# Kernel optimization log

Measured on AMD Instinct MI355X. Metric: run time of the kernel, lower is better.

Reference implementation:

```python
import jax, jax.numpy as jnp
import numpy as np

D_MODEL = 1024
H = 16
D_K = D_MODEL // H
NEG = -1e9


def setup_inputs() -> dict:
    key = jax.random.key(0)
    ks = jax.random.split(key, 12)
    B, S = 4, 2048
    scale = 1.0 / np.sqrt(D_MODEL)
    return {
        "q": jax.random.normal(ks[0], (B, S, D_MODEL), dtype=jnp.float32),
        "k": jax.random.normal(ks[1], (B, S, D_MODEL), dtype=jnp.float32),
        "v": jax.random.normal(ks[2], (B, S, D_MODEL), dtype=jnp.float32),
        "mask": jnp.ones((1, 1, S, S), dtype=jnp.int32),
        "w_q": jax.random.normal(ks[3], (D_MODEL, D_MODEL), dtype=jnp.float32) * scale,
        "b_q": jnp.zeros((D_MODEL,), dtype=jnp.float32),
        "w_k": jax.random.normal(ks[4], (D_MODEL, D_MODEL), dtype=jnp.float32) * scale,
        "b_k": jnp.zeros((D_MODEL,), dtype=jnp.float32),
        "w_v": jax.random.normal(ks[5], (D_MODEL, D_MODEL), dtype=jnp.float32) * scale,
        "b_v": jnp.zeros((D_MODEL,), dtype=jnp.float32),
        "w_o": jax.random.normal(ks[6], (D_MODEL, D_MODEL), dtype=jnp.float32) * scale,
        "b_o": jnp.zeros((D_MODEL,), dtype=jnp.float32),
    }


def reference(q, k, v, mask, w_q, b_q, w_k, b_k, w_v, b_v, w_o, b_o):
    B, S, _ = q.shape
    # projections (torch Linear: x @ W^T + b)
    query = q @ w_q.T + b_q
    key = k @ w_k.T + b_k
    value = v @ w_v.T + b_v
    # [B, S, D] -> [B, H, S, d_k]
    query = query.reshape(B, S, H, D_K).transpose(0, 2, 1, 3)
    key = key.reshape(B, S, H, D_K).transpose(0, 2, 1, 3)
    value = value.reshape(B, S, H, D_K).transpose(0, 2, 1, 3)
    # scaled dot-product attention, full [B,H,S,S] scores as in original
    scores = jnp.einsum("bhqd,bhkd->bhqk", query, key) / jnp.sqrt(
        jnp.asarray(D_K, dtype=query.dtype)
    )
    scores = jnp.where(mask == 0, jnp.asarray(NEG, dtype=scores.dtype), scores)
    attn = jax.nn.softmax(scores, axis=-1)
    x = jnp.einsum("bhqk,bhkd->bhqd", attn, value)
    # [B, H, S, d_k] -> [B, S, D]
    x = x.transpose(0, 2, 1, 3).reshape(B, S, H * D_K)
    return x @ w_o.T + b_o
```

## Files before the change

kernel.cpp:

```cpp
#include <hip/hip_runtime.h>

typedef unsigned short u16;
typedef unsigned int u32;
typedef unsigned long long u64;
typedef __attribute__((ext_vector_type(8))) short short8;
typedef __attribute__((ext_vector_type(4))) float f32x4;
typedef __attribute__((ext_vector_type(16))) float f32x16;
typedef __attribute__((ext_vector_type(4))) u32 u32x4;

constexpr int S_LEN = 2048;
constexpr int DMODEL = 1024;

#if __has_builtin(__builtin_amdgcn_exp2f)
#define EXP2 __builtin_amdgcn_exp2f
#else
#define EXP2 exp2f
#endif

__device__ __forceinline__ u16 f2bf(float f) {
  u32 u = __builtin_bit_cast(u32, f);
  u += 0x7FFFu + ((u >> 16) & 1u);
  return (u16)(u >> 16);
}

__device__ __forceinline__ u32 cvtpk(float a, float b) {
  u32 r;
  asm("v_cvt_pk_bf16_f32 %0, %1, %2" : "=v"(r) : "v"(a), "v"(b));
  return r;
}

__device__ __forceinline__ void plswap(u32& a, u32& b) {
  asm("v_permlane32_swap_b32 %0, %1" : "+v"(a), "+v"(b));
}

__device__ __forceinline__ void gload_lds16(const void* g, void* l) {
  __builtin_amdgcn_global_load_lds((const __attribute__((address_space(1))) u32*)g,
                                   (__attribute__((address_space(3))) u32*)l,
                                   16, 0, 0);
}

__global__ __launch_bounds__(256) void prep_kernel(
    const float* __restrict__ w0, const float* __restrict__ w1,
    const float* __restrict__ w2, const float* __restrict__ w3,
    u16* __restrict__ o0, u16* __restrict__ o1,
    u16* __restrict__ o2, u16* __restrict__ o3,
    const int* __restrict__ mask, u64* __restrict__ mb) {
  if (blockIdx.y == 4) {
    int gw = (blockIdx.x * 256 + threadIdx.x) >> 6;
    int lane = threadIdx.x & 63;
    #pragma unroll
    for (int i = 0; i < 16; ++i) {
      size_t word = (size_t)gw * 16 + i;
      int m = mask[word * 64 + lane];
      u64 bits = __ballot(m != 0);
      if (lane == 0) mb[word] = bits;
    }
    return;
  }
  const float* src; u16* dst;
  switch (blockIdx.y) {
    case 0: src = w0; dst = o0; break;
    case 1: src = w1; dst = o1; break;
    case 2: src = w2; dst = o2; break;
    default: src = w3; dst = o3; break;
  }
  int i = blockIdx.x * 256 + threadIdx.x;
  float4 v = ((const float4*)src)[i];
  ushort4 h;
  h.x = f2bf(v.x); h.y = f2bf(v.y); h.z = f2bf(v.z); h.w = f2bf(v.w);
  ((ushort4*)dst)[i] = h;
}

__global__ __launch_bounds__(256) void cvt_a3_kernel(
    const float* __restrict__ s0, const float* __restrict__ s1,
    const float* __restrict__ s2,
    u16* __restrict__ d0, u16* __restrict__ d1, u16* __restrict__ d2) {
  const float* src; u16* dst;
  switch (blockIdx.y) {
    case 0: src = s0; dst = d0; break;
    case 1: src = s1; dst = d1; break;
    default: src = s2; dst = d2; break;
  }
  int i = blockIdx.x * 256 + threadIdx.x;
  float4 v = ((const float4*)src)[i];
  ushort4 h;
  h.x = f2bf(v.x); h.y = f2bf(v.y); h.z = f2bf(v.z); h.w = f2bf(v.w);
  ((ushort4*)dst)[i] = h;
}

template<int OM>
__global__ __launch_bounds__(256) void gemm_bt_kernel(
    const u16* __restrict__ A, const u16* __restrict__ W,
    const float* __restrict__ bias, void* __restrict__ Cv, float scale) {
  constexpr int BK = 32;
  __shared__ __align__(16) u16 As[128 * BK];
  __shared__ __align__(16) u16 Bs[128 * BK];
  const int tid = threadIdx.x;
  const int lane = tid & 63, w = tid >> 6;
  const int l15 = lane & 15, lg = lane >> 4;
  const int m0 = blockIdx.x * 128, n0 = blockIdx.y * 128;
  const int wm = w >> 1, wn = w & 1;
  f32x4 acc[4][4] = {};

  for (int kt = 0; kt < 1024; kt += BK) {
    #pragma unroll
    for (int j = 0; j < 2; ++j) {
      int sb = (w * 2 + j) * 64;
      int slot = sb + lane;
      int row = slot >> 2, c8 = slot & 3;
      gload_lds16(W + (size_t)(n0 + row) * 1024 + kt + c8 * 8,
                  (char*)Bs + (size_t)sb * 16);
      gload_lds16(A + (size_t)(m0 + row) * 1024 + kt + c8 * 8,
                  (char*)As + (size_t)sb * 16);
    }
    __syncthreads();
    short8 af[4], bfr[4];
    #pragma unroll
    for (int m = 0; m < 4; ++m)
      af[m] = *(const short8*)&As[(wm * 64 + m * 16 + l15) * BK + lg * 8];
    #pragma unroll
    for (int n = 0; n < 4; ++n)
      bfr[n] = *(const short8*)&Bs[(wn * 64 + n * 16 + l15) * BK + lg * 8];
    #pragma unroll
    for (int m = 0; m < 4; ++m)
      #pragma unroll
      for (int n = 0; n < 4; ++n)
        acc[m][n] = __builtin_amdgcn_mfma_f32_16x16x32_bf16(af[m], bfr[n], acc[m][n], 0, 0, 0);
    __syncthreads();
  }

  #pragma unroll
  for (int m = 0; m < 4; ++m) {
    #pragma unroll
    for (int n = 0; n < 4; ++n) {
      int col = n0 + wn * 64 + n * 16 + l15;
      float bcol = bias[col];
      int row0 = m0 + wm * 64 + m * 16 + lg * 4;
      if constexpr (OM == 2) {
        int b = row0 >> 11, s = row0 & 2047;
        ushort4 o;
        o.x = f2bf((acc[m][n][0] + bcol) * scale);
        o.y = f2bf((acc[m][n][1] + bcol) * scale);
        o.z = f2bf((acc[m][n][2] + bcol) * scale);
        o.w = f2bf((acc[m][n][3] + bcol) * scale);
        u16* dst = (u16*)Cv + ((size_t)(b * 16 + (col >> 6)) * 64 + (col & 63)) * S_LEN + s;
        *(ushort4*)dst = o;
      } else {
        #pragma unroll
        for (int r = 0; r < 4; ++r) {
          float v = (acc[m][n][r] + bcol) * scale;
          if constexpr (OM == 1)
            ((float*)Cv)[(size_t)(row0 + r) * 1024 + col] = v;
          else
            ((u16*)Cv)[(size_t)(row0 + r) * 1024 + col] = f2bf(v);
        }
      }
    }
  }
}

__global__ __launch_bounds__(256, 4) void attn_kernel(
    const u16* __restrict__ Qp, const u16* __restrict__ Kp,
    const u16* __restrict__ VpT, const u64* __restrict__ mb,
    u16* __restrict__ X) {
  constexpr float NEGL2 = -1.4426950e9f;
  __shared__ __align__(16) u16 Ks[2][4096];
  __shared__ __align__(16) u16 VTs[2][4096];
  const int tid = threadIdx.x;
  const int lane = tid & 63, w = tid >> 6;
  const int l31 = lane & 31, hi1 = lane >> 5;

  u32 id = blockIdx.x;
  u32 nid = ((id & 7) << 7) | (id >> 3);
  const int bh = nid >> 4, qt = nid & 15;
  const int b = bh >> 4, h = bh & 15;
  const size_t bS = (size_t)b * S_LEN;
  const int wq0 = qt * 128 + w * 32;

  short8 qf[4];
  {
    const u16* qb = Qp + (bS + wq0 + l31) * DMODEL + h * 64;
    #pragma unroll
    for (int dk = 0; dk < 4; ++dk)
      qf[dk] = *(const short8*)(qb + dk * 16 + hi1 * 8);
  }

  f32x16 xacc[2] = {};
  float lsum = 0.f;

  auto stage = [&](int k0, int nb) {
    #pragma unroll
    for (int i = 0; i < 2; ++i) {
      int g = tid + i * 256;
      int kk = g >> 3, dh = g & 7;
      gload_lds16(Kp + (bS + k0 + kk) * DMODEL + h * 64 + ((dh ^ (kk & 7)) << 3),
                  (char*)&Ks[nb][0] + g * 16);
    }
    #pragma unroll
    for (int i = 0; i < 2; ++i) {
      int g = tid + i * 256;
      int dd = g >> 3, kh = g & 7;
      gload_lds16(VpT + ((size_t)(bh * 64 + dd)) * S_LEN + k0 + ((kh ^ (dd & 7)) << 3),
                  (char*)&VTs[nb][0] + g * 16);
    }
  };

  stage(0, 0);
  __syncthreads();

  constexpr int NT = S_LEN / 64;
  for (int t = 0; t < NT; ++t) {
    const int cur = t & 1;
    if (t + 1 < NT) stage((t + 1) * 64, cur ^ 1);

    f32x16 c0, c1;
    #pragma unroll
    for (int r = 0; r < 16; ++r) { c0[r] = -16.f; c1[r] = -16.f; }
    const u16* ksp = &Ks[cur][0];
    __builtin_amdgcn_s_setprio(1);
    #pragma unroll
    for (int dk = 0; dk < 4; ++dk) {
      short8 a0 = *(const short8*)&ksp[((l31) * 64 + dk * 16 + hi1 * 8) ^ ((l31 & 7) << 3)];
      short8 a1 = *(const short8*)&ksp[((32 + l31) * 64 + dk * 16 + hi1 * 8) ^ ((l31 & 7) << 3)];
      c0 = __builtin_amdgcn_mfma_f32_32x32x16_bf16(a0, qf[dk], c0, 0, 0, 0);
      c1 = __builtin_amdgcn_mfma_f32_32x32x16_bf16(a1, qf[dk], c1, 0, 0, 0);
    }
    __builtin_amdgcn_s_setprio(0);

    u64 mw = mb[(size_t)(wq0 + l31) * 32 + t];
    bool allone = __all((long long)mw == -1LL);
    if (!allone) {
      #pragma unroll
      for (int r = 0; r < 16; ++r) {
        int k0i = (r & 3) + 8 * (r >> 2) + 4 * hi1;
        c0[r] = ((mw >> k0i) & 1) ? c0[r] : NEGL2;
        c1[r] = ((mw >> (k0i + 32)) & 1) ? c1[r] : NEGL2;
      }
    }

    float ls = 0.f;
    #pragma unroll
    for (int r = 0; r < 16; ++r) { float p = EXP2(c0[r]); c0[r] = p; ls += p; }
    #pragma unroll
    for (int r = 0; r < 16; ++r) { float p = EXP2(c1[r]); c1[r] = p; ls += p; }
    lsum += ls;

    u32 Wp[2][8];
    #pragma unroll
    for (int i = 0; i < 8; ++i) {
      Wp[0][i] = cvtpk(c0[2 * i], c0[2 * i + 1]);
      Wp[1][i] = cvtpk(c1[2 * i], c1[2 * i + 1]);
    }

    const u16* vtp = &VTs[cur][0];
    __builtin_amdgcn_s_setprio(1);
    #pragma unroll
    for (int ks16 = 0; ks16 < 4; ++ks16) {
      const int kc = ks16 >> 1, ks = ks16 & 1;
      u32 wa0 = Wp[kc][ks * 4 + 0], wb0 = Wp[kc][ks * 4 + 2];
      u32 wa1 = Wp[kc][ks * 4 + 1], wb1 = Wp[kc][ks * 4 + 3];
      plswap(wa0, wb0);
      plswap(wa1, wb1);
      u32x4 pw; pw.x = wa0; pw.y = wa1; pw.z = wb0; pw.w = wb1;
      short8 pfrag = __builtin_bit_cast(short8, pw);
      #pragma unroll
      for (int dt = 0; dt < 2; ++dt) {
        int d = dt * 32 + l31;
        short8 vf = *(const short8*)&vtp[(d * 64 + ks16 * 16 + hi1 * 8) ^ ((d & 7) << 3)];
        xacc[dt] = __builtin_amdgcn_mfma_f32_32x32x16_bf16(vf, pfrag, xacc[dt], 0, 0, 0);
      }
    }
    __builtin_amdgcn_s_setprio(0);
    __syncthreads();
  }

  lsum += __shfl_xor(lsum, 32);
  float inv = 1.0f / lsum;
  u16* xb = X + (bS + wq0 + l31) * DMODEL + h * 64;
  #pragma unroll
  for (int dt = 0; dt < 2; ++dt)
    #pragma unroll
    for (int m = 0; m < 4; ++m) {
      ushort4 o;
      o.x = f2bf(xacc[dt][m * 4 + 0] * inv);
      o.y = f2bf(xacc[dt][m * 4 + 1] * inv);
      o.z = f2bf(xacc[dt][m * 4 + 2] * inv);
      o.w = f2bf(xacc[dt][m * 4 + 3] * inv);
      *(ushort4*)(xb + dt * 32 + m * 8 + hi1 * 4) = o;
    }
}

extern "C" void kernel_launch(void* const* d_in, const int* in_sizes, int n_in,
                              void* d_out, int out_size, void* d_ws, size_t ws_size,
                              hipStream_t stream) {
  const float* q  = (const float*)d_in[0];
  const float* k  = (const float*)d_in[1];
  const float* v  = (const float*)d_in[2];
  const int* mask = (const int*)d_in[3];
  const float* wq = (const float*)d_in[4];
  const float* bq = (const float*)d_in[5];
  const float* wk = (const float*)d_in[6];
  const float* bk = (const float*)d_in[7];
  const float* wv = (const float*)d_in[8];
  const float* bv = (const float*)d_in[9];
  const float* wo = (const float*)d_in[10];
  const float* bo = (const float*)d_in[11];

  char* ws = (char*)d_ws;
  u16* wqb = (u16*)(ws + 0x000000);
  u16* wkb = (u16*)(ws + 0x200000);
  u16* wvb = (u16*)(ws + 0x400000);
  u16* wob = (u16*)(ws + 0x600000);
  u64* mbp = (u64*)(ws + 0x800000);
  u16* Qp  = (u16*)(ws + 0x880000);
  u16* Kp  = (u16*)(ws + 0x1880000);
  u16* Abv = (u16*)(ws + 0x2880000);
  u16* Xp  = (u16*)(ws + 0x3880000);
  u16* VpT = (u16*)(ws + 0x4880000);

  const float QSCALE = 0.125f * 1.44269504088896340736f;
  u16* Abk = (u16*)d_out;
  u16* Abq = Xp;

  prep_kernel<<<dim3(1024, 5), 256, 0, stream>>>(wq, wk, wv, wo, wqb, wkb, wvb, wob,
                                                 mask, mbp);
  cvt_a3_kernel<<<dim3(8192, 3), 256, 0, stream>>>(v, k, q, Abv, Abk, Abq);

  gemm_bt_kernel<2><<<dim3(64, 8), 256, 0, stream>>>(Abv, wvb, bv, VpT, 1.0f);
  gemm_bt_kernel<0><<<dim3(64, 8), 256, 0, stream>>>(Abk, wkb, bk, Kp, 1.0f);
  gemm_bt_kernel<0><<<dim3(64, 8), 256, 0, stream>>>(Abq, wqb, bq, Qp, QSCALE);

  attn_kernel<<<1024, 256, 0, stream>>>(Qp, Kp, VpT, mbp, Xp);
  gemm_bt_kernel<1><<<dim3(64, 8), 256, 0, stream>>>(Xp, wob, bo, (float*)d_out, 1.0f);
}
```

Before: 237.6 us.

## Fuse fp32-to-bf16 activation conversion into projection GEMMs and enlarge attention blocks

Drops the separate activation conversion kernel. The Q/K/V projection GEMMs now load fp32 rows into swizzled LDS and convert them to bf16 while building MFMA fragments, which removes a full write and re-read of the converted activations. The attention kernel moves to 512-thread blocks covering 256 query rows each, so every staged K/V tile is shared by twice as many waves, and the exp sum is split into two accumulators. The trade-off is twice the LDS footprint and bandwidth for the A tile, with conversion work repeated in every N-tile block, and the larger attention blocks may reduce occupancy.

```diff
diff --git a/kernel.cpp b/kernel.cpp
--- a/kernel.cpp
+++ b/kernel.cpp
@@ -71,29 +71,12 @@
   ((ushort4*)dst)[i] = h;
 }
 
-__global__ __launch_bounds__(256) void cvt_a3_kernel(
-    const float* __restrict__ s0, const float* __restrict__ s1,
-    const float* __restrict__ s2,
-    u16* __restrict__ d0, u16* __restrict__ d1, u16* __restrict__ d2) {
-  const float* src; u16* dst;
-  switch (blockIdx.y) {
-    case 0: src = s0; dst = d0; break;
-    case 1: src = s1; dst = d1; break;
-    default: src = s2; dst = d2; break;
-  }
-  int i = blockIdx.x * 256 + threadIdx.x;
-  float4 v = ((const float4*)src)[i];
-  ushort4 h;
-  h.x = f2bf(v.x); h.y = f2bf(v.y); h.z = f2bf(v.z); h.w = f2bf(v.w);
-  ((ushort4*)dst)[i] = h;
-}
-
-template<int OM>
+template<int OM, bool AF32>
 __global__ __launch_bounds__(256) void gemm_bt_kernel(
-    const u16* __restrict__ A, const u16* __restrict__ W,
+    const void* __restrict__ Av, const u16* __restrict__ W,
     const float* __restrict__ bias, void* __restrict__ Cv, float scale) {
   constexpr int BK = 32;
-  __shared__ __align__(16) u16 As[128 * BK];
+  __shared__ __align__(16) char Araw[AF32 ? 128 * BK * 4 : 128 * BK * 2];
   __shared__ __align__(16) u16 Bs[128 * BK];
   const int tid = threadIdx.x;
   const int lane = tid & 63, w = tid >> 6;
@@ -109,15 +92,46 @@
       int slot = sb + lane;
       int row = slot >> 2, c8 = slot & 3;
       gload_lds16(W + (size_t)(n0 + row) * 1024 + kt + c8 * 8,
-                  (char*)Bs + (size_t)sb * 16);
-      gload_lds16(A + (size_t)(m0 + row) * 1024 + kt + c8 * 8,
-                  (char*)As + (size_t)sb * 16);
+                  Bs + (size_t)sb * 8);
+    }
+    if constexpr (AF32) {
+      const float* Af = (const float*)Av;
+      #pragma unroll
+      for (int i = 0; i < 4; ++i) {
+        int g = tid + i * 256;
+        int row = g >> 3;
+        int off16 = (g & 7) ^ (row & 7);
+        gload_lds16(Af + (size_t)(m0 + row) * 1024 + kt + off16 * 4,
+                    Araw + (size_t)g * 16);
+      }
+    } else {
+      const u16* Ab = (const u16*)Av;
+      #pragma unroll
+      for (int j = 0; j < 2; ++j) {
+        int sb = (w * 2 + j) * 64;
+        int slot = sb + lane;
+        int row = slot >> 2, c8 = slot & 3;
+        gload_lds16(Ab + (size_t)(m0 + row) * 1024 + kt + c8 * 8,
+                    Araw + (size_t)slot * 16);
+      }
     }
     __syncthreads();
     short8 af[4], bfr[4];
     #pragma unroll
-    for (int m = 0; m < 4; ++m)
-      af[m] = *(const short8*)&As[(wm * 64 + m * 16 + l15) * BK + lg * 8];
+    for (int m = 0; m < 4; ++m) {
+      int row = wm * 64 + m * 16 + l15;
+      if constexpr (AF32) {
+        const char* rp = Araw + row * 128;
+        float4 fa0 = *(const float4*)(rp + ((lg * 32) ^ ((row & 7) << 4)));
+        float4 fa1 = *(const float4*)(rp + ((lg * 32 + 16) ^ ((row & 7) << 4)));
+        u32x4 pw;
+        pw.x = cvtpk(fa0.x, fa0.y); pw.y = cvtpk(fa0.z, fa0.w);
+        pw.z = cvtpk(fa1.x, fa1.y); pw.w = cvtpk(fa1.z, fa1.w);
+        af[m] = __builtin_bit_cast(short8, pw);
+      } else {
+        af[m] = *(const short8*)&((const u16*)Araw)[row * BK + lg * 8];
+      }
+    }
     #pragma unroll
     for (int n = 0; n < 4; ++n)
       bfr[n] = *(const short8*)&Bs[(wn * 64 + n * 16 + l15) * BK + lg * 8];
@@ -159,7 +173,7 @@
   }
 }
 
-__global__ __launch_bounds__(256, 4) void attn_kernel(
+__global__ __launch_bounds__(512, 4) void attn_kernel(
     const u16* __restrict__ Qp, const u16* __restrict__ Kp,
     const u16* __restrict__ VpT, const u64* __restrict__ mb,
     u16* __restrict__ X) {
@@ -171,11 +185,11 @@
   const int l31 = lane & 31, hi1 = lane >> 5;
 
   u32 id = blockIdx.x;
-  u32 nid = ((id & 7) << 7) | (id >> 3);
-  const int bh = nid >> 4, qt = nid & 15;
+  u32 nid = ((id & 7) << 6) | (id >> 3);
+  const int bh = nid >> 3, qt = nid & 7;
   const int b = bh >> 4, h = bh & 15;
   const size_t bS = (size_t)b * S_LEN;
-  const int wq0 = qt * 128 + w * 32;
+  const int wq0 = qt * 256 + w * 32;
 
   short8 qf[4];
   {
@@ -189,16 +203,14 @@
   float lsum = 0.f;
 
   auto stage = [&](int k0, int nb) {
-    #pragma unroll
-    for (int i = 0; i < 2; ++i) {
-      int g = tid + i * 256;
+    {
+      int g = tid;
       int kk = g >> 3, dh = g & 7;
       gload_lds16(Kp + (bS + k0 + kk) * DMODEL + h * 64 + ((dh ^ (kk & 7)) << 3),
                   (char*)&Ks[nb][0] + g * 16);
     }
-    #pragma unroll
-    for (int i = 0; i < 2; ++i) {
-      int g = tid + i * 256;
+    {
+      int g = tid;
       int dd = g >> 3, kh = g & 7;
       gload_lds16(VpT + ((size_t)(bh * 64 + dd)) * S_LEN + k0 + ((kh ^ (dd & 7)) << 3),
                   (char*)&VTs[nb][0] + g * 16);
@@ -238,12 +250,18 @@
       }
     }
 
-    float ls = 0.f;
-    #pragma unroll
-    for (int r = 0; r < 16; ++r) { float p = EXP2(c0[r]); c0[r] = p; ls += p; }
-    #pragma unroll
-    for (int r = 0; r < 16; ++r) { float p = EXP2(c1[r]); c1[r] = p; ls += p; }
-    lsum += ls;
+    float lsa = 0.f, lsb = 0.f;
+    #pragma unroll
+    for (int r = 0; r < 16; ++r) {
+      float p = EXP2(c0[r]); c0[r] = p;
+      if (r & 1) lsb += p; else lsa += p;
+    }
+    #pragma unroll
+    for (int r = 0; r < 16; ++r) {
+      float p = EXP2(c1[r]); c1[r] = p;
+      if (r & 1) lsb += p; else lsa += p;
+    }
+    lsum += lsa + lsb;
 
     u32 Wp[2][8];
     #pragma unroll
@@ -314,22 +332,18 @@
   u64* mbp = (u64*)(ws + 0x800000);
   u16* Qp  = (u16*)(ws + 0x880000);
   u16* Kp  = (u16*)(ws + 0x1880000);
-  u16* Abv = (u16*)(ws + 0x2880000);
   u16* Xp  = (u16*)(ws + 0x3880000);
   u16* VpT = (u16*)(ws + 0x4880000);
 
   const float QSCALE = 0.125f * 1.44269504088896340736f;
-  u16* Abk = (u16*)d_out;
-  u16* Abq = Xp;
 
   prep_kernel<<<dim3(1024, 5), 256, 0, stream>>>(wq, wk, wv, wo, wqb, wkb, wvb, wob,
                                                  mask, mbp);
-  cvt_a3_kernel<<<dim3(8192, 3), 256, 0, stream>>>(v, k, q, Abv, Abk, Abq);
-
-  gemm_bt_kernel<2><<<dim3(64, 8), 256, 0, stream>>>(Abv, wvb, bv, VpT, 1.0f);
-  gemm_bt_kernel<0><<<dim3(64, 8), 256, 0, stream>>>(Abk, wkb, bk, Kp, 1.0f);
-  gemm_bt_kernel<0><<<dim3(64, 8), 256, 0, stream>>>(Abq, wqb, bq, Qp, QSCALE);
-
-  attn_kernel<<<1024, 256, 0, stream>>>(Qp, Kp, VpT, mbp, Xp);
-  gemm_bt_kernel<1><<<dim3(64, 8), 256, 0, stream>>>(Xp, wob, bo, (float*)d_out, 1.0f);
-}
+
+  gemm_bt_kernel<2, true><<<dim3(64, 8), 256, 0, stream>>>(v, wvb, bv, VpT, 1.0f);
+  gemm_bt_kernel<0, true><<<dim3(64, 8), 256, 0, stream>>>(k, wkb, bk, Kp, 1.0f);
+  gemm_bt_kernel<0, true><<<dim3(64, 8), 256, 0, stream>>>(q, wqb, bq, Qp, QSCALE);
+
+  attn_kernel<<<512, 512, 0, stream>>>(Qp, Kp, VpT, mbp, Xp);
+  gemm_bt_kernel<1, false><<<dim3(64, 8), 256, 0, stream>>>(Xp, wob, bo, (float*)d_out, 1.0f);
+}
```

Result: slower. 270.0 us (+13.7%).
